# Kernel tuning notes

Measured on AMD Instinct MI355X. Metric: run time of the kernel, lower is better.

The kernel has to match this reference:

```python
import jax, jax.numpy as jnp
from jax import lax
import numpy as np

WINDOW_SIZES = (1, 2, 3)


def _proj(x, w1, b1, w2, b2):
    # gated projection: sigmoid(Linear1) * tanh(Linear2)
    return jax.nn.sigmoid(x @ w1.T + b1) * jnp.tanh(x @ w2.T + b2)


def setup_inputs() -> dict:
    key = jax.random.key(0)
    ks = jax.random.split(key, 16)
    V, E, D = 50000, 1024, 1024
    N, La, Lq = 64, 512, 64
    s = 0.02  # weight scale to keep sigmoid/tanh unsaturated
    return {
        "data_q": jax.random.randint(ks[0], (Lq,), 0, V),
        "data_as": jax.random.randint(ks[1], (N, La), 0, V),
        "emb": jax.random.normal(ks[2], (V, E), jnp.float32),
        "w1": jax.random.normal(ks[3], (D, E), jnp.float32) * s,
        "b1": jnp.zeros((D,), jnp.float32),
        "w2": jax.random.normal(ks[4], (D, E), jnp.float32) * s,
        "b2": jnp.zeros((D,), jnp.float32),
        "cw1": jax.random.normal(ks[5], (D, D, 1), jnp.float32) * s,
        "cb1": jnp.zeros((D,), jnp.float32),
        "cw2": jax.random.normal(ks[6], (D, D, 2), jnp.float32) * s,
        "cb2": jnp.zeros((D,), jnp.float32),
        "cw3": jax.random.normal(ks[7], (D, D, 3), jnp.float32) * s,
        "cb3": jnp.zeros((D,), jnp.float32),
        "lin_w": jax.random.normal(ks[8], (D, 3 * D), jnp.float32) * s,
        "lin_b": jnp.zeros((D,), jnp.float32),
        "soft_w": jax.random.normal(ks[9], (1, D), jnp.float32) * s,
        "soft_b": jnp.zeros((1,), jnp.float32),
    }


def reference(data_q, data_as, emb, w1, b1, w2, b2,
              cw1, cb1, cw2, cb2, cw3, cb3, lin_w, lin_b, soft_w, soft_b):
    N, La = data_as.shape
    a_tok = data_as.reshape(-1)                     # [T] concatenated answers
    emb_a = emb[a_tok]                              # [T, E]
    emb_q = emb[data_q]                             # [Lq, E]
    pa = _proj(emb_a, w1, b1, w2, b2)               # [T, D]
    pq = _proj(emb_q, w1, b1, w2, b2)               # [Lq, D]

    # attention: M_r = q @ a^T ; alpha = softmax over question positions
    M = pq @ pa.T                                   # [Lq, T]
    alpha = jax.nn.softmax(M.T, axis=1)             # [T, Lq]
    Y = alpha @ pq                                  # [T, D]
    sim = pa * Y                                    # elementwise compare (mul)

    starts = jnp.arange(N) * La
    x = sim.T[None]                                 # [1, D, T]
    pools = []
    for w, cw, cb in zip(WINDOW_SIZES, (cw1, cw2, cw3), (cb1, cb2, cb3)):
        conv = lax.conv_general_dilated(
            x, cw, (1,), 'VALID',
            dimension_numbers=('NCW', 'OIW', 'NCW'))[0].T + cb  # [T-w+1, D]
        conv = jax.nn.relu(conv)
        # DMax: per-answer max over rows [start_k, start_k + La - w + 1)
        idx = starts[:, None] + jnp.arange(La - w + 1)[None, :]  # [N, La-w+1]
        pools.append(conv[idx].max(axis=1))          # [N, D]

    cat = jnp.concatenate(pools, axis=1)            # [N, 3D]
    h = jnp.tanh(cat @ lin_w.T + lin_b)             # [N, D]
    logits = (h @ soft_w.T + soft_b).reshape(-1)    # [N]
    return jax.nn.log_softmax(logits)
```

## Files before the change

kernel.cpp:

```cpp
#include <hip/hip_runtime.h>

#define DEV __device__ __forceinline__

typedef __bf16 bf16x8 __attribute__((ext_vector_type(8)));
typedef float f32x4 __attribute__((ext_vector_type(4)));
typedef unsigned short u16;
typedef u16 u16x4 __attribute__((ext_vector_type(4)));

constexpr int T_ANS = 32768;
constexpr int LQ    = 64;
constexpr int M_ALL = T_ANS + LQ;
constexpr int M_PAD = 33024;
constexpr int DIM   = 1024;

DEV u16 f2bf(float x) {
  unsigned u = __float_as_uint(x);
  return (u16)((u + 0x7FFFu + ((u >> 16) & 1u)) >> 16);
}
DEV float bf2f(u16 s) { return __uint_as_float(((unsigned)s) << 16); }

DEV void gl2lds16(const void* g, void* l) {
  __builtin_amdgcn_global_load_lds(
      (const __attribute__((address_space(1))) unsigned int*)g,
      (__attribute__((address_space(3))) unsigned int*)l, 16, 0, 0);
}

#define MF(A, B, C) __builtin_amdgcn_mfma_f32_16x16x32_bf16(A, B, C, 0, 0, 0)
#define LFC(P, OFF) (*(const bf16x8*)((P) + (OFF)))


#define STG(G, LT, R0) gl2lds16((G) + (R0) * 2048 + gOff, (LT) + (R0) * 64 + ldOff)

#define S_TILE(AT, BT, BUF)                                                           \
  { const char* ga_ = (AT); const char* gb_ = (BT); char* lb_ = (BUF);                \
    STG(ga_, lb_, 0); STG(ga_, lb_, 128);                                             \
    STG(gb_, lb_ + 16384, 0); STG(gb_, lb_ + 16384, 128); }

#define VMC4 asm volatile("s_waitcnt vmcnt(4)" ::: "memory");
#define VMC0 asm volatile("s_waitcnt vmcnt(0)" ::: "memory");

#define TILEV3(BUF, STAGES, WAIT)                                                     \
  {                                                                                   \
    STAGES                                                                            \
    const char* Ar = (BUF) + rdA;                                                     \
    const char* Br = (BUF) + 16384 + rdB;                                             \
    bf16x8 a0 = LFC(Ar, 0),    a1 = LFC(Ar, 1024), a2 = LFC(Ar, 2048), a3 = LFC(Ar, 3072); \
    bf16x8 a4 = LFC(Ar, 4096), a5 = LFC(Ar, 5120), a6 = LFC(Ar, 6144), a7 = LFC(Ar, 7168); \
    bf16x8 c0 = LFC(Br, 0), c1 = LFC(Br, 1024), c2 = LFC(Br, 2048), c3 = LFC(Br, 3072);    \
    acc[0][0] = MF(a0, c0, acc[0][0]); acc[0][1] = MF(a0, c1, acc[0][1]);             \
    acc[0][2] = MF(a0, c2, acc[0][2]); acc[0][3] = MF(a0, c3, acc[0][3]);             \
    acc[1][0] = MF(a1, c0, acc[1][0]); acc[1][1] = MF(a1, c1, acc[1][1]);             \
    acc[1][2] = MF(a1, c2, acc[1][2]); acc[1][3] = MF(a1, c3, acc[1][3]);             \
    acc[2][0] = MF(a2, c0, acc[2][0]); acc[2][1] = MF(a2, c1, acc[2][1]);             \
    acc[2][2] = MF(a2, c2, acc[2][2]); acc[2][3] = MF(a2, c3, acc[2][3]);             \
    acc[3][0] = MF(a3, c0, acc[3][0]); acc[3][1] = MF(a3, c1, acc[3][1]);             \
    acc[3][2] = MF(a3, c2, acc[3][2]); acc[3][3] = MF(a3, c3, acc[3][3]);             \
    acc[4][0] = MF(a4, c0, acc[4][0]); acc[4][1] = MF(a4, c1, acc[4][1]);             \
    acc[4][2] = MF(a4, c2, acc[4][2]); acc[4][3] = MF(a4, c3, acc[4][3]);             \
    acc[5][0] = MF(a5, c0, acc[5][0]); acc[5][1] = MF(a5, c1, acc[5][1]);             \
    acc[5][2] = MF(a5, c2, acc[5][2]); acc[5][3] = MF(a5, c3, acc[5][3]);             \
    acc[6][0] = MF(a6, c0, acc[6][0]); acc[6][1] = MF(a6, c1, acc[6][1]);             \
    acc[6][2] = MF(a6, c2, acc[6][2]); acc[6][3] = MF(a6, c3, acc[6][3]);             \
    acc[7][0] = MF(a7, c0, acc[7][0]); acc[7][1] = MF(a7, c1, acc[7][1]);             \
    acc[7][2] = MF(a7, c2, acc[7][2]); acc[7][3] = MF(a7, c3, acc[7][3]);             \
    WAIT                                                                              \
    asm volatile("s_barrier" ::: "memory");                                           \
  }

#define GEMM_V3(NT)                                                                   \
  f32x4 acc[8][4] = {};                                                               \
  const int ldOff = tid * 16;                                                         \
  const int gOff = (tid >> 2) * 2048 + (((tid & 3) ^ ((tid >> 2) & 3)) << 4);         \
  const int blk_ = (((lane >> 4) ^ (lane & 3)) << 4);                                 \
  const int rdA = (wm + (lane & 15)) * 64 + blk_;                                     \
  const int rdB = (wn + (lane & 15)) * 64 + blk_;                                     \
  char* b0_ = lds; char* b1_ = lds + 32768; char* b2_ = lds + 65536; char* b3_ = lds + 98304; \
  S_TILE(Ab(0), Bb(0), b0_) S_TILE(Ab(1), Bb(1), b1_)                                 \
  VMC4                                                                                \
  asm volatile("s_barrier" ::: "memory");                                             \
  for (int g = 0; g < (NT) / 4 - 1; ++g) {                                            \
    const int t = 4 * g;                                                              \
    TILEV3(b0_, S_TILE(Ab(t + 2), Bb(t + 2), b2_), VMC4)                              \
    TILEV3(b1_, S_TILE(Ab(t + 3), Bb(t + 3), b3_), VMC4)                              \
    TILEV3(b2_, S_TILE(Ab(t + 4), Bb(t + 4), b0_), VMC4)                              \
    TILEV3(b3_, S_TILE(Ab(t + 5), Bb(t + 5), b1_), VMC4)                              \
  }                                                                                   \
  {                                                                                   \
    const int t = (NT) - 4;                                                           \
    TILEV3(b0_, S_TILE(Ab(t + 2), Bb(t + 2), b2_), VMC4)                              \
    TILEV3(b1_, S_TILE(Ab(t + 3), Bb(t + 3), b3_), VMC4)                              \
    TILEV3(b2_, , VMC0)                                                               \
    TILEV3(b3_, , )                                                                   \
  }


__global__ void cast4(const float* __restrict__ src, u16* __restrict__ dst, int n4) {
  int i = blockIdx.x * 256 + threadIdx.x;
  if (i < n4) {
    float4 v = ((const float4*)src)[i];
    u16x4 o = { f2bf(v.x), f2bf(v.y), f2bf(v.z), f2bf(v.w) };
    ((u16x4*)dst)[i] = o;
  }
}

template<int W>
__global__ void cast_conv_w(const float* __restrict__ src, u16* __restrict__ dst) {
  int i = blockIdx.x * 256 + threadIdx.x;
  if (i < 1024 * 1024) {
#pragma unroll
    for (int k = 0; k < W; ++k)
      dst[(size_t)k * (1024 * 1024) + i] = f2bf(src[(size_t)i * W + k]);
  }
}

__global__ void pack_w12(const float* __restrict__ w1, const float* __restrict__ w2,
                         u16* __restrict__ W12) {
  int i = blockIdx.x * 256 + threadIdx.x;
  if (i < 2048 * 1024) {
    int n2 = i >> 10, k = i & 1023;
    int j = n2 >> 4, m = n2 & 15;
    const float* src = (j & 1) ? w2 : w1;
    W12[i] = f2bf(src[(size_t)((j >> 1) * 16 + m) * 1024 + k]);
  }
}

__global__ void gather_cast(const int* __restrict__ dq, const int* __restrict__ das,
                            const float* __restrict__ emb, u16* __restrict__ X) {
  const int row = blockIdx.x;
  const int c   = threadIdx.x;
  size_t dsto = (size_t)row * DIM + c * 4;
  if (row >= M_ALL) {
    u16x4 z = {0, 0, 0, 0};
    *(u16x4*)(X + dsto) = z;
    return;
  }
  const int tok = (row < T_ANS) ? das[row] : dq[row - T_ANS];
  float4 v = ((const float4*)(emb + (size_t)tok * DIM))[c];
  u16x4 o = { f2bf(v.x), f2bf(v.y), f2bf(v.z), f2bf(v.w) };
  *(u16x4*)(X + dsto) = o;
}

__global__ void transpose_pq(const u16* __restrict__ pa, u16* __restrict__ pqT) {
  int i = blockIdx.x * 256 + threadIdx.x;
  int e = i >> 6, q = i & 63;
  pqT[i] = pa[(size_t)(T_ANS + q) * DIM + e];
}

__global__ void zero_pad_sim(u16* __restrict__ sim) {
  int i = blockIdx.x * 256 + threadIdx.x;
  if (i < 2 * DIM) sim[(size_t)T_ANS * DIM + i] = 0;
}

__global__ void cast_cat(const float* __restrict__ cat, u16* __restrict__ catb) {
  int i = blockIdx.x * 256 + threadIdx.x;
  if (i < 128 * 3072) {
    int row = i / 3072;
    catb[i] = (row < 64) ? f2bf(cat[i]) : (u16)0;
  }
}


__global__ __launch_bounds__(512, 1)
void proj_g(const u16* __restrict__ X, const u16* __restrict__ W12,
            const float* __restrict__ b1, const float* __restrict__ b2,
            u16* __restrict__ pa) {
  extern __shared__ char lds[];
  const int tid = threadIdx.x, lane = tid & 63;
  const int wid = tid >> 6;
  const int wm = (wid >> 2) * 128, wn = (wid & 3) * 64;
  const int lr = lane & 15;
  const int wg = ((int)blockIdx.x % 8) * 129 + (int)blockIdx.x / 8;
  const int tm = (wg >> 3) * 256, tn = (wg & 7) * 256;
  const char* Ag = (const char*)X + (size_t)tm * 2048;
  const char* Bg = (const char*)W12 + (size_t)tn * 2048;
  auto Ab = [&](int t) { return Ag + (t << 6); };
  auto Bb = [&](int t) { return Bg + (t << 6); };

  GEMM_V3(32)

  u16* cw = (u16*)lds;
  const int lg = (lane >> 4) * 4;
#pragma unroll
  for (int pp = 0; pp < 2; ++pp) {
    const int clocal = ((wn >> 5) + pp) * 16 + lr;
    const int col = (tn >> 1) + clocal;
    const float b1v = b1[col], b2v = b2[col];
#pragma unroll
    for (int mi = 0; mi < 8; ++mi)
#pragma unroll
      for (int r = 0; r < 4; ++r) {
        const int rowL = wm + mi * 16 + lg + r;
        const float x1 = acc[mi][2 * pp][r] + b1v;
        const float x2 = acc[mi][2 * pp + 1][r] + b2v;
        const float sg = 1.f / (1.f + __expf(-x1));
        const float th = 2.f / (1.f + __expf(-2.f * x2)) - 1.f;
        cw[rowL * 132 + clocal] = f2bf(sg * th);
      }
  }
  __syncthreads();
#pragma unroll
  for (int it = 0; it < 16; ++it) {
    const int cid = it * 512 + tid;
    const int rowL = cid >> 5, c4 = (cid & 31) * 4;
    u16x4 v = *(const u16x4*)(cw + rowL * 132 + c4);
    *(u16x4*)(pa + (size_t)(tm + rowL) * DIM + (tn >> 1) + c4) = v;
  }
}


template<int W>
__global__ __launch_bounds__(512, 1)
void conv_g(const u16* __restrict__ sim, const u16* __restrict__ Bw,
            const float* __restrict__ cb, float* __restrict__ cat) {
  extern __shared__ char lds[];
  const int tid = threadIdx.x, lane = tid & 63;
  const int wid = tid >> 6;
  const int wm = (wid >> 2) * 128, wn = (wid & 3) * 64;
  const int lr = lane & 15;
  const int wg = ((int)blockIdx.x % 8) * 64 + (int)blockIdx.x / 8;
  const int tm = (wg >> 2) * 256, tn = (wg & 3) * 256;
  const char* Ag = (const char*)sim + (size_t)tm * 2048;
  const char* Bg = (const char*)Bw + (size_t)tn * 2048;
  auto Ab = [&](int t) { return Ag + (t >> 5) * 2048 + ((t & 31) << 6); };
  auto Bb = [&](int t) { return Bg + (size_t)(t >> 5) * 2097152 + ((t & 31) << 6); };

  GEMM_V3(32 * W)

  const int lg = (lane >> 4) * 4;
  const int n = tm >> 9;
#pragma unroll
  for (int ni = 0; ni < 4; ++ni) {
    const int col = tn + wn + ni * 16 + lr;
    const float cbv = cb[col];
    float vmax = 0.f;
#pragma unroll
    for (int mi = 0; mi < 8; ++mi)
#pragma unroll
      for (int r = 0; r < 4; ++r) {
        const int t = tm + wm + mi * 16 + lg + r;
        float v = fmaxf(acc[mi][ni][r] + cbv, 0.f);
        if ((t & 511) > 512 - W) v = 0.f;
        vmax = fmaxf(vmax, v);
      }
    vmax = fmaxf(vmax, __shfl_xor(vmax, 16));
    vmax = fmaxf(vmax, __shfl_xor(vmax, 32));
    if (lane < 16)
      atomicMax((int*)&cat[(size_t)n * 3072 + (W - 1) * 1024 + col], __float_as_int(vmax));
  }
}


__global__ __launch_bounds__(256, 2)
void attn_s(const u16* __restrict__ pa, float* __restrict__ Spart) {
  __shared__ alignas(16) u16 sA[128 * 32];
  __shared__ alignas(16) u16 sB[64 * 32];
  const int tid = threadIdx.x, lane = tid & 63;
  const int tm = blockIdx.x * 128;
  const int kbase = blockIdx.y * 256;
  const int wid = tid >> 6;
  const int wm = (wid >> 1) * 64, wn = (wid & 1) * 32;
  const u16* pq = pa + (size_t)T_ANS * DIM;
  f32x4 acc[4][2] = {};
  for (int k0 = kbase; k0 < kbase + 256; k0 += 32) {
#pragma unroll
    for (int j = 0; j < 2; ++j) {
      const int f = tid * 16 + j * 4096;
      const int r = f >> 6, cb = f & 63;
      gl2lds16((const char*)pa + (size_t)(tm + r) * 2048 + k0 * 2 + cb, (char*)sA + f);
    }
    {
      const int f = tid * 16;
      const int r = f >> 6, cb = f & 63;
      gl2lds16((const char*)pq + (size_t)r * 2048 + k0 * 2 + cb, (char*)sB + f);
    }
    __syncthreads();
    const int lr = lane & 15, lk = (lane >> 4) * 8;
    bf16x8 af[4], bfr[2];
#pragma unroll
    for (int i = 0; i < 4; ++i)
      af[i] = *(const bf16x8*)(sA + (wm + i * 16 + lr) * 32 + lk);
#pragma unroll
    for (int i = 0; i < 2; ++i)
      bfr[i] = *(const bf16x8*)(sB + (wn + i * 16 + lr) * 32 + lk);
#pragma unroll
    for (int mi = 0; mi < 4; ++mi)
#pragma unroll
      for (int ni = 0; ni < 2; ++ni)
        acc[mi][ni] = MF(af[mi], bfr[ni], acc[mi][ni]);
    __syncthreads();
  }
  const int lr = lane & 15, lg = (lane >> 4) * 4;
  float* Sp = Spart + (size_t)blockIdx.y * (T_ANS * 64);
#pragma unroll
  for (int mi = 0; mi < 4; ++mi)
#pragma unroll
    for (int ni = 0; ni < 2; ++ni)
#pragma unroll
      for (int r = 0; r < 4; ++r) {
        const int row = tm + wm + mi * 16 + lg + r;
        const int col = wn + ni * 16 + lr;
        Sp[(size_t)row * 64 + col] = acc[mi][ni][r];
      }
}

__global__ void softmax64(const float* __restrict__ Spart, u16* __restrict__ alpha) {
  const int row = blockIdx.x * 4 + (threadIdx.x >> 6);
  const int lane = threadIdx.x & 63;
  const size_t o = (size_t)row * 64 + lane;
  float v = Spart[o] + Spart[(size_t)1 * T_ANS * 64 + o]
          + Spart[(size_t)2 * T_ANS * 64 + o] + Spart[(size_t)3 * T_ANS * 64 + o];
  float m = v;
#pragma unroll
  for (int o2 = 32; o2 > 0; o2 >>= 1) m = fmaxf(m, __shfl_xor(m, o2));
  const float e = __expf(v - m);
  float s = e;
#pragma unroll
  for (int o2 = 32; o2 > 0; o2 >>= 1) s += __shfl_xor(s, o2);
  alpha[(size_t)row * 64 + lane] = f2bf(e / s);
}


__global__ __launch_bounds__(256, 2)
void attn_y_sim(const u16* __restrict__ alpha, const u16* __restrict__ pqT,
                const u16* __restrict__ pa, u16* __restrict__ sim) {
  __shared__ alignas(16) u16 sA[128 * 32];
  __shared__ alignas(16) u16 sB[128 * 32];
  const int tid = threadIdx.x, lane = tid & 63;
  const int tm = blockIdx.x * 128, tn = blockIdx.y * 128;
  const int wid = tid >> 6;
  const int wm = (wid >> 1) * 64, wn = (wid & 1) * 64;
  f32x4 acc[4][4] = {};
  for (int k0 = 0; k0 < 64; k0 += 32) {
#pragma unroll
    for (int j = 0; j < 2; ++j) {
      const int f = tid * 16 + j * 4096;
      const int r = f >> 6, cb = f & 63;
      gl2lds16((const char*)alpha + (size_t)(tm + r) * 128 + k0 * 2 + cb, (char*)sA + f);
      gl2lds16((const char*)pqT   + (size_t)(tn + r) * 128 + k0 * 2 + cb, (char*)sB + f);
    }
    __syncthreads();
    const int lr = lane & 15, lk = (lane >> 4) * 8;
    bf16x8 af[4], bfr[4];
#pragma unroll
    for (int i = 0; i < 4; ++i) {
      af[i]  = *(const bf16x8*)(sA + (wm + i * 16 + lr) * 32 + lk);
      bfr[i] = *(const bf16x8*)(sB + (wn + i * 16 + lr) * 32 + lk);
    }
#pragma unroll
    for (int mi = 0; mi < 4; ++mi)
#pragma unroll
      for (int ni = 0; ni < 4; ++ni)
        acc[mi][ni] = MF(af[mi], bfr[ni], acc[mi][ni]);
    __syncthreads();
  }
  const int lr = lane & 15, lg = (lane >> 4) * 4;
#pragma unroll
  for (int ni = 0; ni < 4; ++ni) {
    const int col = tn + wn + ni * 16 + lr;
#pragma unroll
    for (int mi = 0; mi < 4; ++mi)
#pragma unroll
      for (int r = 0; r < 4; ++r) {
        const int row = tm + wm + mi * 16 + lg + r;
        const size_t o = (size_t)row * DIM + col;
        sim[o] = f2bf(bf2f(pa[o]) * acc[mi][ni][r]);
      }
  }
}


__global__ __launch_bounds__(256, 2)
void final_h(const u16* __restrict__ catb, const u16* __restrict__ linb,
             const float* __restrict__ lin_b, float* __restrict__ h) {
  __shared__ alignas(16) u16 sA[128 * 32];
  __shared__ alignas(16) u16 sB[128 * 32];
  const int tid = threadIdx.x, lane = tid & 63;
  const int tn = blockIdx.y * 128;
  const int wid = tid >> 6;
  const int wm = (wid >> 1) * 64, wn = (wid & 1) * 64;
  f32x4 acc[4][4] = {};
  for (int k0 = 0; k0 < 3072; k0 += 32) {
#pragma unroll
    for (int j = 0; j < 2; ++j) {
      const int f = tid * 16 + j * 4096;
      const int r = f >> 6, cb = f & 63;
      gl2lds16((const char*)catb + (size_t)r * 6144 + k0 * 2 + cb, (char*)sA + f);
      gl2lds16((const char*)linb + (size_t)(tn + r) * 6144 + k0 * 2 + cb, (char*)sB + f);
    }
    __syncthreads();
    const int lr = lane & 15, lk = (lane >> 4) * 8;
    bf16x8 af[4], bfr[4];
#pragma unroll
    for (int i = 0; i < 4; ++i) {
      af[i]  = *(const bf16x8*)(sA + (wm + i * 16 + lr) * 32 + lk);
      bfr[i] = *(const bf16x8*)(sB + (wn + i * 16 + lr) * 32 + lk);
    }
#pragma unroll
    for (int mi = 0; mi < 4; ++mi)
#pragma unroll
      for (int ni = 0; ni < 4; ++ni)
        acc[mi][ni] = MF(af[mi], bfr[ni], acc[mi][ni]);
    __syncthreads();
  }
  const int lr = lane & 15, lg = (lane >> 4) * 4;
#pragma unroll
  for (int ni = 0; ni < 4; ++ni) {
    const int col = tn + wn + ni * 16 + lr;
    const float bv = lin_b[col];
#pragma unroll
    for (int mi = 0; mi < 4; ++mi)
#pragma unroll
      for (int r = 0; r < 4; ++r) {
        const int row = wm + mi * 16 + lg + r;
        if (row < 64) {
          const float x = acc[mi][ni][r] + bv;
          h[(size_t)row * DIM + col] = 2.f / (1.f + __expf(-2.f * x)) - 1.f;
        }
      }
  }
}

__global__ void final_logits(const float* __restrict__ h, const float* __restrict__ soft_w,
                             const float* __restrict__ soft_b, float* __restrict__ out) {
  __shared__ float part[256];
  const int t = threadIdx.x;
  const int n = t >> 2, q = t & 3;
  float s = 0.f;
  for (int j = q * 256; j < q * 256 + 256; ++j) s += h[(size_t)n * DIM + j] * soft_w[j];
  part[t] = s;
  __syncthreads();
  if (t < 64) {
    float logit = part[t * 4] + part[t * 4 + 1] + part[t * 4 + 2] + part[t * 4 + 3] + soft_b[0];
    float m = logit;
#pragma unroll
    for (int o = 32; o > 0; o >>= 1) m = fmaxf(m, __shfl_xor(m, o));
    float e = __expf(logit - m);
    float ssum = e;
#pragma unroll
    for (int o = 32; o > 0; o >>= 1) ssum += __shfl_xor(ssum, o);
    out[t] = (logit - m) - logf(ssum);
  }
}


extern "C" void kernel_launch(void* const* d_in, const int* in_sizes, int n_in,
                              void* d_out, int out_size, void* d_ws, size_t ws_size,
                              hipStream_t stream) {
  const int*   data_q  = (const int*)d_in[0];
  const int*   data_as = (const int*)d_in[1];
  const float* emb     = (const float*)d_in[2];
  const float* w1      = (const float*)d_in[3];
  const float* b1      = (const float*)d_in[4];
  const float* w2      = (const float*)d_in[5];
  const float* b2      = (const float*)d_in[6];
  const float* cw1     = (const float*)d_in[7];
  const float* cb1     = (const float*)d_in[8];
  const float* cw2     = (const float*)d_in[9];
  const float* cb2     = (const float*)d_in[10];
  const float* cw3     = (const float*)d_in[11];
  const float* cb3     = (const float*)d_in[12];
  const float* lin_w   = (const float*)d_in[13];
  const float* lin_b   = (const float*)d_in[14];
  const float* soft_w  = (const float*)d_in[15];
  const float* soft_b  = (const float*)d_in[16];
  float* out = (float*)d_out;

  hipFuncSetAttribute((const void*)proj_g, hipFuncAttributeMaxDynamicSharedMemorySize, 131072);
  hipFuncSetAttribute((const void*)conv_g<1>, hipFuncAttributeMaxDynamicSharedMemorySize, 131072);
  hipFuncSetAttribute((const void*)conv_g<2>, hipFuncAttributeMaxDynamicSharedMemorySize, 131072);
  hipFuncSetAttribute((const void*)conv_g<3>, hipFuncAttributeMaxDynamicSharedMemorySize, 131072);

  u16* X     = (u16*)d_ws;
  u16* pa    = X    + (size_t)M_PAD * DIM;
  u16* W12   = pa   + (size_t)M_PAD * DIM;
  u16* cwb   = W12  + (size_t)2 * 1024 * 1024;
  u16* linb  = cwb  + (size_t)6 * 1024 * 1024;
  u16* pqT   = linb + (size_t)3 * 1024 * 1024;
  u16* alpha = pqT  + 64 * 1024;
  float* cat = (float*)(alpha + (size_t)T_ANS * 64);
  u16* catb  = (u16*)(cat + 64 * 3072);
  float* h   = (float*)(catb + 128 * 3072);
  u16* simb  = X;
  float* Spart = (float*)X;

  hipMemsetAsync(cat, 0, 64 * 3072 * sizeof(float), stream);

  pack_w12<<<8192, 256, 0, stream>>>(w1, w2, W12);
  cast4<<<3072, 256, 0, stream>>>(lin_w, linb, 3072 * 1024 / 4);
  cast_conv_w<1><<<4096, 256, 0, stream>>>(cw1, cwb);
  cast_conv_w<2><<<4096, 256, 0, stream>>>(cw2, cwb + (size_t)1 * 1024 * 1024);
  cast_conv_w<3><<<4096, 256, 0, stream>>>(cw3, cwb + (size_t)3 * 1024 * 1024);

  gather_cast<<<M_PAD, 256, 0, stream>>>(data_q, data_as, emb, X);

  proj_g<<<1032, 512, 131072, stream>>>(X, W12, b1, b2, pa);
  transpose_pq<<<256, 256, 0, stream>>>(pa, pqT);

  attn_s<<<dim3(T_ANS / 128, 4), 256, 0, stream>>>(pa, Spart);
  softmax64<<<T_ANS / 4, 256, 0, stream>>>(Spart, alpha);
  attn_y_sim<<<dim3(T_ANS / 128, 8), 256, 0, stream>>>(alpha, pqT, pa, simb);
  zero_pad_sim<<<8, 256, 0, stream>>>(simb);

  conv_g<1><<<512, 512, 131072, stream>>>(simb, cwb, cb1, cat);
  conv_g<2><<<512, 512, 131072, stream>>>(simb, cwb + (size_t)1 * 1024 * 1024, cb2, cat);
  conv_g<3><<<512, 512, 131072, stream>>>(simb, cwb + (size_t)3 * 1024 * 1024, cb3, cat);

  cast_cat<<<1536, 256, 0, stream>>>(cat, catb);
  final_h<<<dim3(1, 8), 256, 0, stream>>>(catb, linb, lin_b, h);
  final_logits<<<1, 256, 0, stream>>>(h, soft_w, soft_b, out);
}
```

Baseline: 773.4 us.

## Replace tuned projection GEMM with simple 128x128 single-buffered tile kernel

The gated projection GEMM drops the pipelined 256x256 GEMM_V3 macro with 512 threads and large dynamic LDS. It uses a plain 128x128 tile with 256 threads, static 16 KB LDS, and a load/sync/compute/sync loop with no double buffering. The epilogue now writes bf16 results straight to global memory, one scalar at a time, instead of staging them in LDS for vector stores. This likely serves as a simpler baseline or allows more occupancy, but it gives up data reuse, overlap of loads with compute, and coalesced stores.

```diff
diff --git a/kernel.cpp b/kernel.cpp
--- a/kernel.cpp
+++ b/kernel.cpp
@@ -160,50 +160,57 @@
 }
 
 
-__global__ __launch_bounds__(512, 1)
+__global__ __launch_bounds__(256)
 void proj_g(const u16* __restrict__ X, const u16* __restrict__ W12,
             const float* __restrict__ b1, const float* __restrict__ b2,
             u16* __restrict__ pa) {
-  extern __shared__ char lds[];
+  __shared__ alignas(16) u16 sA[128 * 32];
+  __shared__ alignas(16) u16 sB[128 * 32];
   const int tid = threadIdx.x, lane = tid & 63;
   const int wid = tid >> 6;
-  const int wm = (wid >> 2) * 128, wn = (wid & 3) * 64;
-  const int lr = lane & 15;
-  const int wg = ((int)blockIdx.x % 8) * 129 + (int)blockIdx.x / 8;
-  const int tm = (wg >> 3) * 256, tn = (wg & 7) * 256;
-  const char* Ag = (const char*)X + (size_t)tm * 2048;
-  const char* Bg = (const char*)W12 + (size_t)tn * 2048;
-  auto Ab = [&](int t) { return Ag + (t << 6); };
-  auto Bb = [&](int t) { return Bg + (t << 6); };
-
-  GEMM_V3(32)
-
-  u16* cw = (u16*)lds;
-  const int lg = (lane >> 4) * 4;
-#pragma unroll
-  for (int pp = 0; pp < 2; ++pp) {
-    const int clocal = ((wn >> 5) + pp) * 16 + lr;
-    const int col = (tn >> 1) + clocal;
+  const int wm = (wid >> 1) * 64, wn = (wid & 1) * 64;
+  const int wg = ((int)blockIdx.x % 8) * 516 + (int)blockIdx.x / 8;
+  const int tm = (wg >> 4) * 128, tn = (wg & 15) * 128;
+  f32x4 acc[4][4] = {};
+  for (int k0 = 0; k0 < 1024; k0 += 32) {
+#pragma unroll
+    for (int j = 0; j < 2; ++j) {
+      const int f = tid * 16 + j * 4096;
+      const int r = f >> 6, cb = f & 63;
+      gl2lds16((const char*)X   + (size_t)(tm + r) * 2048 + k0 * 2 + cb, (char*)sA + f);
+      gl2lds16((const char*)W12 + (size_t)(tn + r) * 2048 + k0 * 2 + cb, (char*)sB + f);
+    }
+    __syncthreads();
+    const int lr = lane & 15, lk = (lane >> 4) * 8;
+    bf16x8 af[4], bf[4];
+#pragma unroll
+    for (int i = 0; i < 4; ++i) {
+      af[i] = *(const bf16x8*)(sA + (wm + i * 16 + lr) * 32 + lk);
+      bf[i] = *(const bf16x8*)(sB + (wn + i * 16 + lr) * 32 + lk);
+    }
+#pragma unroll
+    for (int mi = 0; mi < 4; ++mi)
+#pragma unroll
+      for (int ni = 0; ni < 4; ++ni)
+        acc[mi][ni] = MF(af[mi], bf[ni], acc[mi][ni]);
+    __syncthreads();
+  }
+  const int lr = lane & 15, lg = (lane >> 4) * 4;
+#pragma unroll
+  for (int np = 0; np < 2; ++np) {
+    const int col = ((tn + wn) >> 1) + np * 16 + lr;
     const float b1v = b1[col], b2v = b2[col];
 #pragma unroll
-    for (int mi = 0; mi < 8; ++mi)
+    for (int mi = 0; mi < 4; ++mi)
 #pragma unroll
       for (int r = 0; r < 4; ++r) {
-        const int rowL = wm + mi * 16 + lg + r;
-        const float x1 = acc[mi][2 * pp][r] + b1v;
-        const float x2 = acc[mi][2 * pp + 1][r] + b2v;
+        const int row = tm + wm + mi * 16 + lg + r;
+        const float x1 = acc[mi][2 * np][r] + b1v;
+        const float x2 = acc[mi][2 * np + 1][r] + b2v;
         const float sg = 1.f / (1.f + __expf(-x1));
         const float th = 2.f / (1.f + __expf(-2.f * x2)) - 1.f;
-        cw[rowL * 132 + clocal] = f2bf(sg * th);
+        pa[(size_t)row * DIM + col] = f2bf(sg * th);
       }
-  }
-  __syncthreads();
-#pragma unroll
-  for (int it = 0; it < 16; ++it) {
-    const int cid = it * 512 + tid;
-    const int rowL = cid >> 5, c4 = (cid & 31) * 4;
-    u16x4 v = *(const u16x4*)(cw + rowL * 132 + c4);
-    *(u16x4*)(pa + (size_t)(tm + rowL) * DIM + (tn >> 1) + c4) = v;
   }
 }
 
@@ -465,7 +472,6 @@
   const float* soft_b  = (const float*)d_in[16];
   float* out = (float*)d_out;
 
-  hipFuncSetAttribute((const void*)proj_g, hipFuncAttributeMaxDynamicSharedMemorySize, 131072);
   hipFuncSetAttribute((const void*)conv_g<1>, hipFuncAttributeMaxDynamicSharedMemorySize, 131072);
   hipFuncSetAttribute((const void*)conv_g<2>, hipFuncAttributeMaxDynamicSharedMemorySize, 131072);
   hipFuncSetAttribute((const void*)conv_g<3>, hipFuncAttributeMaxDynamicSharedMemorySize, 131072);
@@ -493,7 +499,7 @@
 
   gather_cast<<<M_PAD, 256, 0, stream>>>(data_q, data_as, emb, X);
 
-  proj_g<<<1032, 512, 131072, stream>>>(X, W12, b1, b2, pa);
+  proj_g<<<4128, 256, 0, stream>>>(X, W12, b1, b2, pa);
   transpose_pq<<<256, 256, 0, stream>>>(pa, pqT);
 
   attn_s<<<dim3(T_ANS / 128, 4), 256, 0, stream>>>(pa, Spart);
```

Measured after the change: 759.1 us. Within noise of the previous version (-1.9%).
